# Performance work log

Hardware: AMD Instinct MI355X
Metric: run time of the kernel (lower is better)

## Reference

```python
import jax, jax.numpy as jnp
import numpy as np

B, T, H, P = 512, 256, 256, 14  # batch, seq_len, hidden_size, predict_seq


def _lstm_layer(x_tbf, w_ih, w_hh, b_ih, b_hh):
    """One LSTM layer. x_tbf: [T, B, F]. Returns outputs [T, B, H].
    PyTorch gate order: i, f, g, o."""
    # Precompute input contribution for all timesteps: [T, B, 4H]
    pre = jnp.einsum('tbf,gf->tbg', x_tbf, w_ih) + b_ih + b_hh
    h0 = jnp.zeros((x_tbf.shape[1], w_hh.shape[1]), dtype=x_tbf.dtype)
    c0 = jnp.zeros_like(h0)

    def step(carry, pre_t):
        h, c = carry
        gates = pre_t + h @ w_hh.T                      # [B, 4H]
        i, f, g, o = jnp.split(gates, 4, axis=-1)
        i = jax.nn.sigmoid(i)
        f = jax.nn.sigmoid(f)
        g = jnp.tanh(g)
        o = jax.nn.sigmoid(o)
        c = f * c + i * g
        h = o * jnp.tanh(c)
        return (h, c), h

    _, ys = jax.lax.scan(step, (h0, c0), pre)
    return ys  # [T, B, H]


def setup_inputs() -> dict:
    key = jax.random.key(0)
    ks = jax.random.split(key, 11)
    s = 1.0 / np.sqrt(H)  # torch LSTM/Linear default init scale
    return {
        'x':     jax.random.normal(ks[0], (B, T, 1), dtype=jnp.float32),
        'w_ih0': jax.random.uniform(ks[1], (4 * H, 1), jnp.float32, -s, s),
        'w_hh0': jax.random.uniform(ks[2], (4 * H, H), jnp.float32, -s, s),
        'b_ih0': jax.random.uniform(ks[3], (4 * H,), jnp.float32, -s, s),
        'b_hh0': jax.random.uniform(ks[4], (4 * H,), jnp.float32, -s, s),
        'w_ih1': jax.random.uniform(ks[5], (4 * H, H), jnp.float32, -s, s),
        'w_hh1': jax.random.uniform(ks[6], (4 * H, H), jnp.float32, -s, s),
        'b_ih1': jax.random.uniform(ks[7], (4 * H,), jnp.float32, -s, s),
        'b_hh1': jax.random.uniform(ks[8], (4 * H,), jnp.float32, -s, s),
        'w_lin': jax.random.uniform(ks[9], (P, H), jnp.float32, -s, s),
        'b_lin': jax.random.uniform(ks[10], (P,), jnp.float32, -s, s),
    }


def reference(x, w_ih0, w_hh0, b_ih0, b_hh0, w_ih1, w_hh1, b_ih1, b_hh1,
              w_lin, b_lin):
    xt = jnp.transpose(x, (1, 0, 2))                 # [T, B, 1]
    h1 = _lstm_layer(xt, w_ih0, w_hh0, b_ih0, b_hh0)  # [T, B, H]
    h2 = _lstm_layer(h1, w_ih1, w_hh1, b_ih1, b_hh1)  # [T, B, H]
    last = h2[-1]                                     # [B, H] == x[:, -1, :]
    return last @ w_lin.T + b_lin                     # [B, P]
```

## Files before the change

### kernel.cpp

```cpp
#include <hip/hip_runtime.h>

constexpr int Bz = 512;
constexpr int Tz = 256;
constexpr int Hz = 256;
constexpr int Pz = 14;
constexpr int GB = 32;
constexpr int GS = 8;
constexpr int BT = 16;
constexpr int KP = 264;
constexpr int XS = 260;

typedef short s8v __attribute__((ext_vector_type(8)));
typedef float f4v __attribute__((ext_vector_type(4)));
typedef unsigned long long u64;

__device__ __forceinline__ short f2bf(float f) {
  unsigned u = __float_as_uint(f);
  u = (u + 0x7fffu + ((u >> 16) & 1u)) >> 16;
  return (short)u;
}
__device__ __forceinline__ float bf2f(short s) {
  return __uint_as_float(((unsigned)(unsigned short)s) << 16);
}
__device__ __forceinline__ float sigm(float v) { return 1.0f / (1.0f + __expf(-v)); }
__device__ __forceinline__ float tanh_f(float v) { return 1.0f - 2.0f / (__expf(2.0f * v) + 1.0f); }

__device__ __forceinline__ u64 llc_load64(const u64* p) {
  return __hip_atomic_load(p, __ATOMIC_RELAXED, __HIP_MEMORY_SCOPE_AGENT);
}
__device__ __forceinline__ unsigned llc_load32(const unsigned* p) {
  return __hip_atomic_load(p, __ATOMIC_RELAXED, __HIP_MEMORY_SCOPE_AGENT);
}
__device__ __forceinline__ void llc_store32(unsigned* p, unsigned v) {
  __hip_atomic_store(p, v, __ATOMIC_RELAXED, __HIP_MEMORY_SCOPE_AGENT);
}

__global__ void __launch_bounds__(256, 1)
lstm2(const float* __restrict__ x,
      const float* __restrict__ w_ih0, const float* __restrict__ w_hh0,
      const float* __restrict__ b_ih0, const float* __restrict__ b_hh0,
      const float* __restrict__ w_ih1, const float* __restrict__ w_hh1,
      const float* __restrict__ b_ih1, const float* __restrict__ b_hh1,
      const float* __restrict__ w_lin, const float* __restrict__ b_lin,
      float* __restrict__ out,
      unsigned* __restrict__ h0g, unsigned* __restrict__ h1g,
      unsigned* __restrict__ flags)
{
  const int blk  = blockIdx.x;
  const int g    = blk >> 3;
  const int sl   = blk & 7;
  const int tid  = threadIdx.x;
  const int w    = tid >> 6;
  const int lane = tid & 63;
  const int q    = lane >> 4;
  const int l15  = lane & 15;
  const int gbase = g * BT;

  extern __shared__ char smem_raw[];
  short* h0s = (short*)smem_raw;
  short* h1s = h0s + BT * KP;
  float* xls = (float*)(h1s + BT * KP);
  float* wls = xls + BT * XS;

  s8v Wf[3][2][8];
  {
    const float* wsrc[3] = {w_hh0, w_ih1, w_hh1};
    #pragma unroll
    for (int mat = 0; mat < 3; ++mat) {
      #pragma unroll
      for (int mti = 0; mti < 2; ++mti) {
        int rr = (w + mti * 4) * 16 + l15;
        int grow = (rr & 3) * Hz + sl * 32 + (rr >> 2);
        const float* p = wsrc[mat] + (size_t)grow * Hz;
        #pragma unroll
        for (int kt = 0; kt < 8; ++kt) {
          s8v f;
          #pragma unroll
          for (int j = 0; j < 8; ++j) {
            int ktrue = kt * 32 + q * 4 + (j >> 1) + 16 * (j & 1);
            f[j] = f2bf(p[ktrue]);
          }
          Wf[mat][mti][kt] = f;
        }
      }
    }
  }
  const int uA = w * 4 + q, uB = 16 + w * 4 + q;
  float wihA[4], wihB[4], b0A[4], b0B[4], b1A[4], b1B[4];
  #pragma unroll
  for (int r = 0; r < 4; ++r) {
    int ga_ = r * Hz + sl * 32 + uA;
    int gb_ = r * Hz + sl * 32 + uB;
    wihA[r] = w_ih0[ga_];              wihB[r] = w_ih0[gb_];
    b0A[r]  = b_ih0[ga_] + b_hh0[ga_]; b0B[r]  = b_ih0[gb_] + b_hh0[gb_];
    b1A[r]  = b_ih1[ga_] + b_hh1[ga_]; b1B[r]  = b_ih1[gb_] + b_hh1[gb_];
  }
  float c0A = 0.f, c0B = 0.f, c1A = 0.f, c1B = 0.f;

  for (int i = tid; i < BT * (Tz / 4); i += 256) {
    int b = i >> 6, c4 = i & 63;
    f4v v = *(const f4v*)(x + (size_t)(gbase + b) * Tz + c4 * 4);
    *(f4v*)(xls + b * XS + c4 * 4) = v;
  }
  if (sl == 0) {
    for (int i = tid; i < Pz * Hz; i += 256) {
      int p = i >> 8, kpos = i & 255;
      int sl2 = kpos >> 5, w2 = (kpos >> 3) & 3, q2 = (kpos >> 1) & 3, jj = kpos & 1;
      wls[i] = w_lin[p * Hz + sl2 * 32 + w2 * 4 + q2 + 16 * jj];
    }
  }

  const unsigned* myflags = flags + g * 32 + (lane & 7);
  unsigned* myflag = flags + g * 32 + sl;

  for (int s = 0; s <= Tz; ++s) {
    {
      const unsigned expd = (unsigned)s;
      unsigned f = llc_load32(myflags);
      while (__ballot(f >= expd) != ~0ull) {
        __builtin_amdgcn_s_sleep(1);
        f = llc_load32(myflags);
      }
    }

    {
      const u64* s0 = (const u64*)h0g + (size_t)((s + 1) & 1) * 32768;
      const u64* s1 = (const u64*)h1g + (size_t)(s & 1) * 32768;
      u64 r0[4], r1[4];
      #pragma unroll
      for (int k = 0; k < 4; ++k) {
        int i = tid + k * 256;
        int c = i & 1, b = (i >> 1) & 15, slw = i >> 5;
        size_t gi = ((size_t)slw * Bz + gbase + b) * 2 + c;
        r0[k] = llc_load64(s0 + gi);
        r1[k] = llc_load64(s1 + gi);
      }
      #pragma unroll
      for (int k = 0; k < 4; ++k) {
        int i = tid + k * 256;
        int c = i & 1, b = (i >> 1) & 15, slw = i >> 5;
        *(u64*)(h0s + b * KP + slw * 8 + c * 4) = r0[k];
        *(u64*)(h1s + b * KP + slw * 8 + c * 4) = r1[k];
      }
    }
    __syncthreads();

    f4v a0A = {0.f,0.f,0.f,0.f}, a0B = {0.f,0.f,0.f,0.f};
    f4v a1A = {0.f,0.f,0.f,0.f}, a1B = {0.f,0.f,0.f,0.f};
    const short* H0f = h0s + l15 * KP + q * 8;
    const short* H1f = h1s + l15 * KP + q * 8;
    #pragma unroll
    for (int kt = 0; kt < 8; ++kt) {
      s8v h0v = *(const s8v*)(H0f + kt * 32);
      s8v h1v = *(const s8v*)(H1f + kt * 32);
      a0A = __builtin_amdgcn_mfma_f32_16x16x32_bf16(Wf[0][0][kt], h0v, a0A, 0, 0, 0);
      a0B = __builtin_amdgcn_mfma_f32_16x16x32_bf16(Wf[0][1][kt], h0v, a0B, 0, 0, 0);
      a1A = __builtin_amdgcn_mfma_f32_16x16x32_bf16(Wf[1][0][kt], h0v, a1A, 0, 0, 0);
      a1B = __builtin_amdgcn_mfma_f32_16x16x32_bf16(Wf[1][1][kt], h0v, a1B, 0, 0, 0);
      a1A = __builtin_amdgcn_mfma_f32_16x16x32_bf16(Wf[2][0][kt], h1v, a1A, 0, 0, 0);
      a1B = __builtin_amdgcn_mfma_f32_16x16x32_bf16(Wf[2][1][kt], h1v, a1B, 0, 0, 0);
    }

    unsigned pk0 = 0, pk1 = 0;
    if (s < Tz) {
      float xv = xls[l15 * XS + s];
      float iA = sigm  (a0A[0] + xv * wihA[0] + b0A[0]);
      float fA = sigm  (a0A[1] + xv * wihA[1] + b0A[1]);
      float gA = tanh_f(a0A[2] + xv * wihA[2] + b0A[2]);
      float oA = sigm  (a0A[3] + xv * wihA[3] + b0A[3]);
      c0A = fA * c0A + iA * gA;
      float iB = sigm  (a0B[0] + xv * wihB[0] + b0B[0]);
      float fB = sigm  (a0B[1] + xv * wihB[1] + b0B[1]);
      float gB = tanh_f(a0B[2] + xv * wihB[2] + b0B[2]);
      float oB = sigm  (a0B[3] + xv * wihB[3] + b0B[3]);
      c0B = fB * c0B + iB * gB;
      pk0 = (unsigned)(unsigned short)f2bf(oA * tanh_f(c0A))
          | ((unsigned)(unsigned short)f2bf(oB * tanh_f(c0B)) << 16);
    }
    if (s >= 1) {
      float iA = sigm  (a1A[0] + b1A[0]);
      float fA = sigm  (a1A[1] + b1A[1]);
      float gA = tanh_f(a1A[2] + b1A[2]);
      float oA = sigm  (a1A[3] + b1A[3]);
      c1A = fA * c1A + iA * gA;
      float iB = sigm  (a1B[0] + b1B[0]);
      float fB = sigm  (a1B[1] + b1B[1]);
      float gB = tanh_f(a1B[2] + b1B[2]);
      float oB = sigm  (a1B[3] + b1B[3]);
      c1B = fB * c1B + iB * gB;
      pk1 = (unsigned)(unsigned short)f2bf(oA * tanh_f(c1A))
          | ((unsigned)(unsigned short)f2bf(oB * tanh_f(c1B)) << 16);
    }

    {
      size_t base = (size_t)(sl * 4 + w) * 2048 + (size_t)(gbase + l15) * 4 + q;
      if (s < Tz)
        llc_store32(h0g + (size_t)(s & 1) * 65536 + base, pk0);
      if (s >= 1)
        llc_store32(h1g + (size_t)((s - 1) & 1) * 65536 + base, pk1);
    }

    __syncthreads();
    if (tid == 0)
      llc_store32(myflag, (unsigned)(s + 1));
  }

  if (sl == 0) {
    {
      const unsigned expd = (unsigned)(Tz + 1);
      unsigned f = llc_load32(myflags);
      while (__ballot(f >= expd) != ~0ull) {
        __builtin_amdgcn_s_sleep(1);
        f = llc_load32(myflags);
      }
    }
    const u64* s1 = (const u64*)h1g + (size_t)((Tz - 1) & 1) * 32768;
    for (int k = 0; k < 4; ++k) {
      int i = tid + k * 256;
      int c = i & 1, b = (i >> 1) & 15, slw = i >> 5;
      u64 v = llc_load64(s1 + ((size_t)slw * Bz + gbase + b) * 2 + c);
      *(u64*)(h0s + b * KP + slw * 8 + c * 4) = v;
    }
    __syncthreads();
    for (int i = tid; i < BT * Pz; i += 256) {
      int b = i / Pz, p = i - b * Pz;
      const float* wr = wls + p * Hz;
      float acc = b_lin[p];
      for (int kk = 0; kk < Hz; ++kk)
        acc += bf2f(h0s[b * KP + kk]) * wr[kk];
      out[(gbase + b) * Pz + p] = acc;
    }
  }
}

extern "C" void kernel_launch(void* const* d_in, const int* in_sizes, int n_in,
                              void* d_out, int out_size, void* d_ws, size_t ws_size,
                              hipStream_t stream) {
  const float* x     = (const float*)d_in[0];
  const float* w_ih0 = (const float*)d_in[1];
  const float* w_hh0 = (const float*)d_in[2];
  const float* b_ih0 = (const float*)d_in[3];
  const float* b_hh0 = (const float*)d_in[4];
  const float* w_ih1 = (const float*)d_in[5];
  const float* w_hh1 = (const float*)d_in[6];
  const float* b_ih1 = (const float*)d_in[7];
  const float* b_hh1 = (const float*)d_in[8];
  const float* w_lin = (const float*)d_in[9];
  const float* b_lin = (const float*)d_in[10];
  float* out = (float*)d_out;

  unsigned char* ws = (unsigned char*)d_ws;
  unsigned* h0g   = (unsigned*)ws;
  unsigned* h1g   = (unsigned*)(ws + (512 << 10));
  unsigned* flags = (unsigned*)(ws + (1024 << 10));
  hipMemsetAsync(d_ws, 0, (1024 << 10) + 4096, stream);

  size_t lds_bytes = (size_t)(2 * BT) * KP * 2
                   + (size_t)(BT * XS) * 4
                   + (size_t)(Pz * Hz) * 4;
  hipFuncSetAttribute((const void*)lstm2,
                      hipFuncAttributeMaxDynamicSharedMemorySize, (int)lds_bytes);
  lstm2<<<GB * GS, 256, lds_bytes, stream>>>(x, w_ih0, w_hh0, b_ih0, b_hh0,
                                             w_ih1, w_hh1, b_ih1, b_hh1,
                                             w_lin, b_lin, out, h0g, h1g, flags);
}
```

Baseline: 800.4 us.

## Split layers across wave pairs with per-wave flag sync and direct fragment loads

Each block now gives waves 0-1 to layer 0 and waves 2-3 to layer 1, so the two layers run concurrently as a wavefront pipeline instead of being computed together in lockstep by every wave. Each wave pair signals its own flag after draining its stores and polls only the flags it depends on, which removes the block-wide __syncthreads barriers from the timestep loop. Hidden-state fragments are loaded straight from global/LLC into MFMA operand registers rather than staged through LDS. The w_hh1 weights move into LDS to free registers, which adds LDS reads inside the layer-1 loop and leaves layer 1 doing twice the MFMA work of layer 0 per step.

```diff
diff --git a/kernel.cpp b/kernel.cpp
--- a/kernel.cpp
+++ b/kernel.cpp
@@ -33,6 +33,20 @@
 }
 __device__ __forceinline__ void llc_store32(unsigned* p, unsigned v) {
   __hip_atomic_store(p, v, __ATOMIC_RELAXED, __HIP_MEMORY_SCOPE_AGENT);
+}
+__device__ __forceinline__ void drain_vm() {
+  asm volatile("s_waitcnt vmcnt(0)" ::: "memory");
+}
+
+__device__ __forceinline__ void poll2(const unsigned* fb, int lane, int e0, int e1) {
+  int idx = lane & 31;
+  const unsigned* p = fb + idx;
+  int expd = (idx < 16) ? e0 : e1;
+  int f = (int)llc_load32(p);
+  while (__ballot(f >= expd) != ~0ull) {
+    __builtin_amdgcn_s_sleep(1);
+    f = (int)llc_load32(p);
+  }
 }
 
 __global__ void __launch_bounds__(256, 1)
@@ -55,47 +69,55 @@
   const int q    = lane >> 4;
   const int l15  = lane & 15;
   const int gbase = g * BT;
+  const int W    = w & 1;
 
   extern __shared__ char smem_raw[];
-  short* h0s = (short*)smem_raw;
-  short* h1s = h0s + BT * KP;
-  float* xls = (float*)(h1s + BT * KP);
+  short* w1l = (short*)smem_raw;
+  float* xls = (float*)(w1l + 128 * KP);
   float* wls = xls + BT * XS;
-
-  s8v Wf[3][2][8];
+  short* hst = (short*)(wls + Pz * Hz);
+
+  s8v WfA[4][8];
   {
-    const float* wsrc[3] = {w_hh0, w_ih1, w_hh1};
+    const float* wsrc = (w < 2) ? w_hh0 : w_ih1;
     #pragma unroll
-    for (int mat = 0; mat < 3; ++mat) {
-      #pragma unroll
-      for (int mti = 0; mti < 2; ++mti) {
-        int rr = (w + mti * 4) * 16 + l15;
-        int grow = (rr & 3) * Hz + sl * 32 + (rr >> 2);
-        const float* p = wsrc[mat] + (size_t)grow * Hz;
+    for (int j4 = 0; j4 < 4; ++j4) {
+      int t = 2 * W + (j4 & 1) + (j4 >> 1) * 4;
+      int rr = t * 16 + l15;
+      int grow = (rr & 3) * Hz + sl * 32 + (rr >> 2);
+      const float* p = wsrc + (size_t)grow * Hz;
+      #pragma unroll
+      for (int kt = 0; kt < 8; ++kt) {
+        s8v f;
         #pragma unroll
-        for (int kt = 0; kt < 8; ++kt) {
-          s8v f;
-          #pragma unroll
-          for (int j = 0; j < 8; ++j) {
-            int ktrue = kt * 32 + q * 4 + (j >> 1) + 16 * (j & 1);
-            f[j] = f2bf(p[ktrue]);
-          }
-          Wf[mat][mti][kt] = f;
+        for (int j = 0; j < 8; ++j) {
+          int ktrue = kt * 32 + q * 4 + (j >> 1) + 16 * (j & 1);
+          f[j] = f2bf(p[ktrue]);
         }
-      }
-    }
-  }
-  const int uA = w * 4 + q, uB = 16 + w * 4 + q;
-  float wihA[4], wihB[4], b0A[4], b0B[4], b1A[4], b1B[4];
+        WfA[j4][kt] = f;
+      }
+    }
+  }
+  for (int i = tid; i < 128 * 256; i += 256) {
+    int r = i >> 8, kpos = i & 255;
+    int grow = (r & 3) * Hz + sl * 32 + (r >> 2);
+    int kt = kpos >> 5, rem = kpos & 31, q2 = rem >> 3, j = rem & 7;
+    int ktrue = kt * 32 + q2 * 4 + (j >> 1) + 16 * (j & 1);
+    w1l[r * KP + kpos] = f2bf(w_hh1[(size_t)grow * Hz + ktrue]);
+  }
+  float wih[4][4], bia[4][4];
   #pragma unroll
-  for (int r = 0; r < 4; ++r) {
-    int ga_ = r * Hz + sl * 32 + uA;
-    int gb_ = r * Hz + sl * 32 + uB;
-    wihA[r] = w_ih0[ga_];              wihB[r] = w_ih0[gb_];
-    b0A[r]  = b_ih0[ga_] + b_hh0[ga_]; b0B[r]  = b_ih0[gb_] + b_hh0[gb_];
-    b1A[r]  = b_ih1[ga_] + b_hh1[ga_]; b1B[r]  = b_ih1[gb_] + b_hh1[gb_];
-  }
-  float c0A = 0.f, c0B = 0.f, c1A = 0.f, c1B = 0.f;
+  for (int j4 = 0; j4 < 4; ++j4) {
+    int t = 2 * W + (j4 & 1) + (j4 >> 1) * 4;
+    int u = t * 4 + q;
+    #pragma unroll
+    for (int r = 0; r < 4; ++r) {
+      int gi = r * Hz + sl * 32 + u;
+      if (w < 2) { wih[j4][r] = w_ih0[gi]; bia[j4][r] = b_ih0[gi] + b_hh0[gi]; }
+      else       { wih[j4][r] = 0.f;       bia[j4][r] = b_ih1[gi] + b_hh1[gi]; }
+    }
+  }
+  float cc[4] = {0.f, 0.f, 0.f, 0.f};
 
   for (int i = tid; i < BT * (Tz / 4); i += 256) {
     int b = i >> 6, c4 = i & 63;
@@ -109,117 +131,117 @@
       wls[i] = w_lin[p * Hz + sl2 * 32 + w2 * 4 + q2 + 16 * jj];
     }
   }
-
-  const unsigned* myflags = flags + g * 32 + (lane & 7);
-  unsigned* myflag = flags + g * 32 + sl;
-
-  for (int s = 0; s <= Tz; ++s) {
-    {
-      const unsigned expd = (unsigned)s;
-      unsigned f = llc_load32(myflags);
-      while (__ballot(f >= expd) != ~0ull) {
-        __builtin_amdgcn_s_sleep(1);
-        f = llc_load32(myflags);
-      }
-    }
-
-    {
-      const u64* s0 = (const u64*)h0g + (size_t)((s + 1) & 1) * 32768;
-      const u64* s1 = (const u64*)h1g + (size_t)(s & 1) * 32768;
-      u64 r0[4], r1[4];
-      #pragma unroll
-      for (int k = 0; k < 4; ++k) {
-        int i = tid + k * 256;
-        int c = i & 1, b = (i >> 1) & 15, slw = i >> 5;
-        size_t gi = ((size_t)slw * Bz + gbase + b) * 2 + c;
-        r0[k] = llc_load64(s0 + gi);
-        r1[k] = llc_load64(s1 + gi);
-      }
-      #pragma unroll
-      for (int k = 0; k < 4; ++k) {
-        int i = tid + k * 256;
-        int c = i & 1, b = (i >> 1) & 15, slw = i >> 5;
-        *(u64*)(h0s + b * KP + slw * 8 + c * 4) = r0[k];
-        *(u64*)(h1s + b * KP + slw * 8 + c * 4) = r1[k];
-      }
-    }
-    __syncthreads();
-
-    f4v a0A = {0.f,0.f,0.f,0.f}, a0B = {0.f,0.f,0.f,0.f};
-    f4v a1A = {0.f,0.f,0.f,0.f}, a1B = {0.f,0.f,0.f,0.f};
-    const short* H0f = h0s + l15 * KP + q * 8;
-    const short* H1f = h1s + l15 * KP + q * 8;
+  __syncthreads();
+
+  const unsigned* fb = flags + g * 64;
+  const size_t fragbase = (size_t)q * 1024 + (size_t)(gbase + l15) * 2;
+  const size_t st0 = (size_t)(sl * 4 + 2 * W) * 2048 + (size_t)(gbase + l15) * 4 + q;
+  const size_t st1 = st0 + 2048;
+
+  if (w < 2) {
+    unsigned* myflag = flags + g * 64 + sl * 2 + W;
+    for (int t = 0; t < Tz; ++t) {
+      poll2(fb, lane, t, t - 1);
+      const u64* src = (const u64*)h0g + (size_t)((t + 1) & 1) * 32768;
+      u64 lo[8], hi[8];
+      #pragma unroll
+      for (int kt = 0; kt < 8; ++kt) {
+        size_t a = fragbase + (size_t)kt * 4096;
+        lo[kt] = llc_load64(src + a);
+        hi[kt] = llc_load64(src + a + 1);
+      }
+      f4v acc[4] = {{0,0,0,0},{0,0,0,0},{0,0,0,0},{0,0,0,0}};
+      #pragma unroll
+      for (int kt = 0; kt < 8; ++kt) {
+        union { u64 d[2]; s8v v; } hv;
+        hv.d[0] = lo[kt]; hv.d[1] = hi[kt];
+        #pragma unroll
+        for (int j4 = 0; j4 < 4; ++j4)
+          acc[j4] = __builtin_amdgcn_mfma_f32_16x16x32_bf16(WfA[j4][kt], hv.v, acc[j4], 0, 0, 0);
+      }
+      float xv = xls[l15 * XS + t];
+      float hh[4];
+      #pragma unroll
+      for (int j4 = 0; j4 < 4; ++j4) {
+        float iv = sigm  (acc[j4][0] + xv * wih[j4][0] + bia[j4][0]);
+        float fv = sigm  (acc[j4][1] + xv * wih[j4][1] + bia[j4][1]);
+        float gv = tanh_f(acc[j4][2] + xv * wih[j4][2] + bia[j4][2]);
+        float ov = sigm  (acc[j4][3] + xv * wih[j4][3] + bia[j4][3]);
+        cc[j4] = fv * cc[j4] + iv * gv;
+        hh[j4] = ov * tanh_f(cc[j4]);
+      }
+      unsigned* dst = h0g + (size_t)(t & 1) * 65536;
+      unsigned pkA = (unsigned)(unsigned short)f2bf(hh[0])
+                   | ((unsigned)(unsigned short)f2bf(hh[2]) << 16);
+      unsigned pkB = (unsigned)(unsigned short)f2bf(hh[1])
+                   | ((unsigned)(unsigned short)f2bf(hh[3]) << 16);
+      llc_store32(dst + st0, pkA);
+      llc_store32(dst + st1, pkB);
+      drain_vm();
+      if (lane == 0) llc_store32(myflag, (unsigned)(t + 1));
+    }
+  } else {
+    unsigned* myflag = flags + g * 64 + 16 + sl * 2 + W;
+    const short* whbase = w1l + l15 * KP + q * 8;
     #pragma unroll
-    for (int kt = 0; kt < 8; ++kt) {
-      s8v h0v = *(const s8v*)(H0f + kt * 32);
-      s8v h1v = *(const s8v*)(H1f + kt * 32);
-      a0A = __builtin_amdgcn_mfma_f32_16x16x32_bf16(Wf[0][0][kt], h0v, a0A, 0, 0, 0);
-      a0B = __builtin_amdgcn_mfma_f32_16x16x32_bf16(Wf[0][1][kt], h0v, a0B, 0, 0, 0);
-      a1A = __builtin_amdgcn_mfma_f32_16x16x32_bf16(Wf[1][0][kt], h0v, a1A, 0, 0, 0);
-      a1B = __builtin_amdgcn_mfma_f32_16x16x32_bf16(Wf[1][1][kt], h0v, a1B, 0, 0, 0);
-      a1A = __builtin_amdgcn_mfma_f32_16x16x32_bf16(Wf[2][0][kt], h1v, a1A, 0, 0, 0);
-      a1B = __builtin_amdgcn_mfma_f32_16x16x32_bf16(Wf[2][1][kt], h1v, a1B, 0, 0, 0);
-    }
-
-    unsigned pk0 = 0, pk1 = 0;
-    if (s < Tz) {
-      float xv = xls[l15 * XS + s];
-      float iA = sigm  (a0A[0] + xv * wihA[0] + b0A[0]);
-      float fA = sigm  (a0A[1] + xv * wihA[1] + b0A[1]);
-      float gA = tanh_f(a0A[2] + xv * wihA[2] + b0A[2]);
-      float oA = sigm  (a0A[3] + xv * wihA[3] + b0A[3]);
-      c0A = fA * c0A + iA * gA;
-      float iB = sigm  (a0B[0] + xv * wihB[0] + b0B[0]);
-      float fB = sigm  (a0B[1] + xv * wihB[1] + b0B[1]);
-      float gB = tanh_f(a0B[2] + xv * wihB[2] + b0B[2]);
-      float oB = sigm  (a0B[3] + xv * wihB[3] + b0B[3]);
-      c0B = fB * c0B + iB * gB;
-      pk0 = (unsigned)(unsigned short)f2bf(oA * tanh_f(c0A))
-          | ((unsigned)(unsigned short)f2bf(oB * tanh_f(c0B)) << 16);
-    }
-    if (s >= 1) {
-      float iA = sigm  (a1A[0] + b1A[0]);
-      float fA = sigm  (a1A[1] + b1A[1]);
-      float gA = tanh_f(a1A[2] + b1A[2]);
-      float oA = sigm  (a1A[3] + b1A[3]);
-      c1A = fA * c1A + iA * gA;
-      float iB = sigm  (a1B[0] + b1B[0]);
-      float fB = sigm  (a1B[1] + b1B[1]);
-      float gB = tanh_f(a1B[2] + b1B[2]);
-      float oB = sigm  (a1B[3] + b1B[3]);
-      c1B = fB * c1B + iB * gB;
-      pk1 = (unsigned)(unsigned short)f2bf(oA * tanh_f(c1A))
-          | ((unsigned)(unsigned short)f2bf(oB * tanh_f(c1B)) << 16);
-    }
-
-    {
-      size_t base = (size_t)(sl * 4 + w) * 2048 + (size_t)(gbase + l15) * 4 + q;
-      if (s < Tz)
-        llc_store32(h0g + (size_t)(s & 1) * 65536 + base, pk0);
-      if (s >= 1)
-        llc_store32(h1g + (size_t)((s - 1) & 1) * 65536 + base, pk1);
-    }
-
-    __syncthreads();
-    if (tid == 0)
-      llc_store32(myflag, (unsigned)(s + 1));
+    for (int dummy = 0; dummy < 1; ++dummy) {}
+    for (int t = 0; t < Tz; ++t) {
+      poll2(fb, lane, t + 1, t);
+      const u64* s0 = (const u64*)h0g + (size_t)(t & 1) * 32768;
+      const u64* s1 = (const u64*)h1g + (size_t)((t + 1) & 1) * 32768;
+      u64 lo0[8], hi0[8], lo1[8], hi1[8];
+      #pragma unroll
+      for (int kt = 0; kt < 8; ++kt) {
+        size_t a = fragbase + (size_t)kt * 4096;
+        lo0[kt] = llc_load64(s0 + a);
+        hi0[kt] = llc_load64(s0 + a + 1);
+        lo1[kt] = llc_load64(s1 + a);
+        hi1[kt] = llc_load64(s1 + a + 1);
+      }
+      f4v acc[4] = {{0,0,0,0},{0,0,0,0},{0,0,0,0},{0,0,0,0}};
+      #pragma unroll
+      for (int kt = 0; kt < 8; ++kt) {
+        union { u64 d[2]; s8v v; } h0v, h1v;
+        h0v.d[0] = lo0[kt]; h0v.d[1] = hi0[kt];
+        h1v.d[0] = lo1[kt]; h1v.d[1] = hi1[kt];
+        #pragma unroll
+        for (int j4 = 0; j4 < 4; ++j4) {
+          int t4 = 2 * W + (j4 & 1) + (j4 >> 1) * 4;
+          s8v wh = *(const s8v*)(whbase + (t4 * 16) * KP + kt * 32);
+          acc[j4] = __builtin_amdgcn_mfma_f32_16x16x32_bf16(WfA[j4][kt], h0v.v, acc[j4], 0, 0, 0);
+          acc[j4] = __builtin_amdgcn_mfma_f32_16x16x32_bf16(wh, h1v.v, acc[j4], 0, 0, 0);
+        }
+      }
+      float hh[4];
+      #pragma unroll
+      for (int j4 = 0; j4 < 4; ++j4) {
+        float iv = sigm  (acc[j4][0] + bia[j4][0]);
+        float fv = sigm  (acc[j4][1] + bia[j4][1]);
+        float gv = tanh_f(acc[j4][2] + bia[j4][2]);
+        float ov = sigm  (acc[j4][3] + bia[j4][3]);
+        cc[j4] = fv * cc[j4] + iv * gv;
+        hh[j4] = ov * tanh_f(cc[j4]);
+      }
+      unsigned* dst = h1g + (size_t)(t & 1) * 65536;
+      unsigned pkA = (unsigned)(unsigned short)f2bf(hh[0])
+                   | ((unsigned)(unsigned short)f2bf(hh[2]) << 16);
+      unsigned pkB = (unsigned)(unsigned short)f2bf(hh[1])
+                   | ((unsigned)(unsigned short)f2bf(hh[3]) << 16);
+      llc_store32(dst + st0, pkA);
+      llc_store32(dst + st1, pkB);
+      drain_vm();
+      if (lane == 0) llc_store32(myflag, (unsigned)(t + 1));
+    }
   }
 
   if (sl == 0) {
-    {
-      const unsigned expd = (unsigned)(Tz + 1);
-      unsigned f = llc_load32(myflags);
-      while (__ballot(f >= expd) != ~0ull) {
-        __builtin_amdgcn_s_sleep(1);
-        f = llc_load32(myflags);
-      }
-    }
+    poll2(fb, lane, Tz, Tz);
     const u64* s1 = (const u64*)h1g + (size_t)((Tz - 1) & 1) * 32768;
     for (int k = 0; k < 4; ++k) {
       int i = tid + k * 256;
       int c = i & 1, b = (i >> 1) & 15, slw = i >> 5;
       u64 v = llc_load64(s1 + ((size_t)slw * Bz + gbase + b) * 2 + c);
-      *(u64*)(h0s + b * KP + slw * 8 + c * 4) = v;
+      *(u64*)(hst + b * KP + slw * 8 + c * 4) = v;
     }
     __syncthreads();
     for (int i = tid; i < BT * Pz; i += 256) {
@@ -227,7 +249,7 @@
       const float* wr = wls + p * Hz;
       float acc = b_lin[p];
       for (int kk = 0; kk < Hz; ++kk)
-        acc += bf2f(h0s[b * KP + kk]) * wr[kk];
+        acc += bf2f(hst[b * KP + kk]) * wr[kk];
       out[(gbase + b) * Pz + p] = acc;
     }
   }
@@ -253,11 +275,12 @@
   unsigned* h0g   = (unsigned*)ws;
   unsigned* h1g   = (unsigned*)(ws + (512 << 10));
   unsigned* flags = (unsigned*)(ws + (1024 << 10));
-  hipMemsetAsync(d_ws, 0, (1024 << 10) + 4096, stream);
-
-  size_t lds_bytes = (size_t)(2 * BT) * KP * 2
+  hipMemsetAsync(d_ws, 0, (1024 << 10) + 16384, stream);
+
+  size_t lds_bytes = (size_t)128 * KP * 2
                    + (size_t)(BT * XS) * 4
-                   + (size_t)(Pz * Hz) * 4;
+                   + (size_t)(Pz * Hz) * 4
+                   + (size_t)BT * KP * 2;
   hipFuncSetAttribute((const void*)lstm2,
                       hipFuncAttributeMaxDynamicSharedMemorySize, (int)lds_bytes);
   lstm2<<<GB * GS, 256, lds_bytes, stream>>>(x, w_ih0, w_hh0, b_ih0, b_hh0,
```

Measured after the change: 1.414 ms. 76.6% more time.
